# Performance work log

Measured on AMD Instinct MI355X. Metric: run time of the kernel, lower is better.

The kernel has to match this reference:

```python
import jax, jax.numpy as jnp
import numpy as np

N_NODES = 50000
N_EDGES = 800000


def _glorot(key, shape):
    fan_in, fan_out = shape
    lim = float(np.sqrt(6.0 / (fan_in + fan_out)))
    return jax.random.uniform(key, shape, jnp.float32, -lim, lim)


def setup_inputs() -> dict:
    key = jax.random.key(0)
    ks = jax.random.split(key, 8)
    x = jax.random.normal(ks[0], (N_NODES, 2), jnp.float32)
    edge_index = jax.random.randint(ks[1], (2, N_EDGES), 0, N_NODES, jnp.int64)
    edge_weight = jax.random.uniform(ks[2], (N_EDGES,), jnp.float32)
    return {
        "x": x,
        "edge_index": edge_index,
        "edge_weight": edge_weight,
        "W1": _glorot(ks[3], (2, 128)),
        "b1": jnp.zeros((128,), jnp.float32),
        "W2": _glorot(ks[4], (128, 64)),
        "b2": jnp.zeros((64,), jnp.float32),
        "W3": _glorot(ks[5], (64, 1)),
        "b3": jnp.zeros((1,), jnp.float32),
    }


def _gcn_conv(x, W, b, src, dst, ew, n_nodes):
    # PyG GCNConv with normalize=False: out[i] = sum_{e:(j->i)} ew[e] * (x_j @ W) + b
    h = x @ W                       # [N, F_out] tiny GEMM
    msg = h[src] * ew[:, None]      # [E, F_out] gather + scale
    out = jax.ops.segment_sum(msg, dst, num_segments=n_nodes)  # scatter-add
    return out + b


def reference(x, edge_index, edge_weight, W1, b1, W2, b2, W3, b3):
    src, dst = edge_index[0], edge_index[1]  # source_to_target flow: aggregate at dst
    n = x.shape[0]
    h1 = jax.nn.relu(_gcn_conv(x, W1, b1, src, dst, edge_weight, n))
    # dropout is a no-op in eval mode
    h2 = jax.nn.relu(_gcn_conv(h1, W2, b2, src, dst, edge_weight, n))
    h3 = _gcn_conv(h2, W3, b3, src, dst, edge_weight, n)  # [N, 1]
    return h3.squeeze(-1)  # [N]
```

## Files before the change

### kernel.cpp

```cpp
#include <hip/hip_runtime.h>
#include <hip/hip_fp16.h>

#define N_NODES 50000
#define N_EDGES 800000
#define BSHIFT 7
#define NBKT ((N_NODES + 127) >> BSHIFT)
#define CAP 3072
#define P1_EDGES 2048
#define P1_BLOCKS ((N_EDGES + P1_EDGES - 1) / P1_EDGES)
#define BIN_THREADS 512
#define SL_THREADS 512

__global__ void bin_edges(const int* __restrict__ src, const int* __restrict__ dst,
                          const float* __restrict__ ew, int* __restrict__ bcur,
                          unsigned* __restrict__ bpk, unsigned char* __restrict__ bdl) {
    __shared__ unsigned spk[P1_EDGES];
    __shared__ unsigned short sdst[P1_EDGES];
    __shared__ int cnt[NBKT];
    __shared__ int cbase[NBKT];
    int t = threadIdx.x;
    if (t < NBKT) cnt[t] = 0;
    __syncthreads();
    int e0 = blockIdx.x * P1_EDGES;
    for (int k = 0; k < P1_EDGES / BIN_THREADS; k++) {
        int i = k * BIN_THREADS + t;
        int e = e0 + i;
        if (e < N_EDGES) {
            int d = dst[e];
            unsigned hw = (unsigned)__half_as_ushort(__float2half(ew[e]));
            spk[i] = (unsigned)src[e] | (hw << 16);
            sdst[i] = (unsigned short)d;
            atomicAdd(&cnt[d >> BSHIFT], 1);
        }
    }
    __syncthreads();
    if (t < NBKT) {
        int v = cnt[t];
        int base = v ? atomicAdd(&bcur[t], v) : 0;
        cbase[t] = t * CAP + base;
        cnt[t] = 0;
    }
    __syncthreads();
    int nmax = N_EDGES - e0;
    if (nmax > P1_EDGES) nmax = P1_EDGES;
    for (int k = 0; k < P1_EDGES / BIN_THREADS; k++) {
        int i = k * BIN_THREADS + t;
        if (i < nmax) {
            int d = sdst[i];
            int b = d >> BSHIFT;
            int pos = cbase[b] + atomicAdd(&cnt[b], 1);
            bpk[pos] = spk[i];
            bdl[pos] = (unsigned char)(d & 127);
        }
    }
}

__device__ __forceinline__ float edge_w(unsigned p) {
    return __half2float(__ushort_as_half((unsigned short)(p >> 16)));
}

typedef _Float16 f16x8 __attribute__((ext_vector_type(8)));
typedef float f32x4 __attribute__((ext_vector_type(4)));

__global__ __launch_bounds__(SL_THREADS) void sort_l1(
    const int* __restrict__ bcur, const unsigned* __restrict__ bpk,
    const unsigned char* __restrict__ bdl, const float* __restrict__ x,
    const float* __restrict__ W1, const float* __restrict__ b1,
    const float* __restrict__ W2,
    unsigned* __restrict__ sorted, int2* __restrict__ rowspan,
    __half* __restrict__ t2) {
    __shared__ unsigned spk[CAP];
    __shared__ unsigned short sdl[CAP];
    __shared__ int nh[128], scn[128], lcur[128];
    __shared__ float nodeA[128], nodeB[128];
    __shared__ __align__(16) __half w2t[64][136];
    __shared__ __align__(16) float w1r0[128];
    __shared__ __align__(16) float w1r1[128];
    __shared__ __align__(16) float b1s[128];

    int b = blockIdx.x;
    int t = threadIdx.x;
    int base = b * CAP;
    int n = bcur[b];
    if (n > CAP) n = CAP;

    for (int idx = t; idx < 128 * 64; idx += SL_THREADS) {
        int k = idx >> 6, nn = idx & 63;
        w2t[nn][k] = __float2half(W2[idx]);
    }
    if (t < 128) {
        w1r0[t] = W1[t];
        w1r1[t] = W1[128 + t];
        b1s[t]  = b1[t];
        nh[t] = 0;
        lcur[t] = 0;
        nodeA[t] = 0.f;
        nodeB[t] = 0.f;
    }
    __syncthreads();

    for (int e = t; e < n; e += SL_THREADS) {
        spk[e] = bpk[base + e];
        unsigned short d = bdl[base + e];
        sdl[e] = d;
        atomicAdd(&nh[d], 1);
    }
    __syncthreads();

    int v = 0;
    if (t < 128) { v = nh[t]; scn[t] = v; }
    __syncthreads();
    for (int off = 1; off < 128; off <<= 1) {
        int u = (t < 128 && t >= off) ? scn[t - off] : 0;
        __syncthreads();
        if (t < 128) scn[t] += u;
        __syncthreads();
    }
    if (t < 128) {
        int ex = scn[t] - v;
        int node = (b << BSHIFT) + t;
        if (node < N_NODES) rowspan[node] = make_int2(base + ex, base + ex + v);
        nh[t] = ex;
    }
    __syncthreads();

    for (int e = t; e < n; e += SL_THREADS) {
        unsigned p = spk[e];
        int dlow = sdl[e];
        int pos = base + nh[dlow] + atomicAdd(&lcur[dlow], 1);
        sorted[pos] = p;
        float w = edge_w(p);
        float2 xv = ((const float2*)x)[p & 0xFFFF];
        atomicAdd(&nodeA[dlow], w * xv.x);
        atomicAdd(&nodeB[dlow], w * xv.y);
    }
    __syncthreads();

    int wave = t >> 6, lane = t & 63;
    int m0 = wave * 16;
    int fr = lane & 15;
    int kb = (lane >> 4) * 8;
    float a0 = nodeA[m0 + fr];
    float a1 = nodeB[m0 + fr];
    f32x4 acc0 = {0.f, 0.f, 0.f, 0.f};
    f32x4 acc1 = {0.f, 0.f, 0.f, 0.f};
    f32x4 acc2 = {0.f, 0.f, 0.f, 0.f};
    f32x4 acc3 = {0.f, 0.f, 0.f, 0.f};
#pragma unroll
    for (int k0 = 0; k0 < 128; k0 += 32) {
        f16x8 av;
#pragma unroll
        for (int j = 0; j < 8; j++) {
            int k = k0 + kb + j;
            float h = fmaxf(fmaf(a0, w1r0[k], fmaf(a1, w1r1[k], b1s[k])), 0.f);
            av[j] = (_Float16)h;
        }
        f16x8 bv0 = *(const f16x8*)&w2t[ 0 + fr][k0 + kb];
        f16x8 bv1 = *(const f16x8*)&w2t[16 + fr][k0 + kb];
        f16x8 bv2 = *(const f16x8*)&w2t[32 + fr][k0 + kb];
        f16x8 bv3 = *(const f16x8*)&w2t[48 + fr][k0 + kb];
        acc0 = __builtin_amdgcn_mfma_f32_16x16x32_f16(av, bv0, acc0, 0, 0, 0);
        acc1 = __builtin_amdgcn_mfma_f32_16x16x32_f16(av, bv1, acc1, 0, 0, 0);
        acc2 = __builtin_amdgcn_mfma_f32_16x16x32_f16(av, bv2, acc2, 0, 0, 0);
        acc3 = __builtin_amdgcn_mfma_f32_16x16x32_f16(av, bv3, acc3, 0, 0, 0);
    }
    int rowb = (b << BSHIFT) + m0 + (lane >> 4) * 4;
#pragma unroll
    for (int r = 0; r < 4; r++) {
        int node = rowb + r;
        if (node < N_NODES) {
            __half* o = t2 + node * 64 + fr;
            o[0]  = __float2half(acc0[r]);
            o[16] = __float2half(acc1[r]);
            o[32] = __float2half(acc2[r]);
            o[48] = __float2half(acc3[r]);
        }
    }
}

__global__ void gather2_dot3(const int2* __restrict__ rowspan, const unsigned* __restrict__ sorted,
                             const __half* __restrict__ t2, const float* __restrict__ b2,
                             const float* __restrict__ W3, float* __restrict__ t3) {
    int gtid = blockIdx.x * blockDim.x + threadIdx.x;
    int node = gtid >> 6;
    int lane = threadIdx.x & 63;
    if (node >= N_NODES) return;
    int eg  = lane >> 3;
    int fli = lane & 7;
    int2 sp = rowspan[node];
    float a0 = 0.f, a1 = 0.f, a2 = 0.f, a3 = 0.f, a4 = 0.f, a5 = 0.f, a6 = 0.f, a7 = 0.f;
    int e = sp.x + eg;
    for (; e + 8 < sp.y; e += 16) {
        unsigned p0 = sorted[e];
        unsigned p1 = sorted[e + 8];
        uint4 q0 = *(const uint4*)(t2 + (p0 & 0xFFFF) * 64 + fli * 8);
        uint4 q1 = *(const uint4*)(t2 + (p1 & 0xFFFF) * 64 + fli * 8);
        float w0 = edge_w(p0), w1 = edge_w(p1);
        float2 f;
        f = __half22float2(*(const __half2*)&q0.x); a0 = fmaf(w0, f.x, a0); a1 = fmaf(w0, f.y, a1);
        f = __half22float2(*(const __half2*)&q0.y); a2 = fmaf(w0, f.x, a2); a3 = fmaf(w0, f.y, a3);
        f = __half22float2(*(const __half2*)&q0.z); a4 = fmaf(w0, f.x, a4); a5 = fmaf(w0, f.y, a5);
        f = __half22float2(*(const __half2*)&q0.w); a6 = fmaf(w0, f.x, a6); a7 = fmaf(w0, f.y, a7);
        f = __half22float2(*(const __half2*)&q1.x); a0 = fmaf(w1, f.x, a0); a1 = fmaf(w1, f.y, a1);
        f = __half22float2(*(const __half2*)&q1.y); a2 = fmaf(w1, f.x, a2); a3 = fmaf(w1, f.y, a3);
        f = __half22float2(*(const __half2*)&q1.z); a4 = fmaf(w1, f.x, a4); a5 = fmaf(w1, f.y, a5);
        f = __half22float2(*(const __half2*)&q1.w); a6 = fmaf(w1, f.x, a6); a7 = fmaf(w1, f.y, a7);
    }
    if (e < sp.y) {
        unsigned p = sorted[e];
        uint4 q = *(const uint4*)(t2 + (p & 0xFFFF) * 64 + fli * 8);
        float w = edge_w(p);
        float2 f;
        f = __half22float2(*(const __half2*)&q.x); a0 = fmaf(w, f.x, a0); a1 = fmaf(w, f.y, a1);
        f = __half22float2(*(const __half2*)&q.y); a2 = fmaf(w, f.x, a2); a3 = fmaf(w, f.y, a3);
        f = __half22float2(*(const __half2*)&q.z); a4 = fmaf(w, f.x, a4); a5 = fmaf(w, f.y, a5);
        f = __half22float2(*(const __half2*)&q.w); a6 = fmaf(w, f.x, a6); a7 = fmaf(w, f.y, a7);
    }
#pragma unroll
    for (int off = 8; off < 64; off <<= 1) {
        a0 += __shfl_xor(a0, off); a1 += __shfl_xor(a1, off);
        a2 += __shfl_xor(a2, off); a3 += __shfl_xor(a3, off);
        a4 += __shfl_xor(a4, off); a5 += __shfl_xor(a5, off);
        a6 += __shfl_xor(a6, off); a7 += __shfl_xor(a7, off);
    }
    float4 bA = *(const float4*)(b2 + fli * 8);
    float4 bB = *(const float4*)(b2 + fli * 8 + 4);
    float4 wA = *(const float4*)(W3 + fli * 8);
    float4 wB = *(const float4*)(W3 + fli * 8 + 4);
    float h = fmaxf(a0 + bA.x, 0.f) * wA.x + fmaxf(a1 + bA.y, 0.f) * wA.y +
              fmaxf(a2 + bA.z, 0.f) * wA.z + fmaxf(a3 + bA.w, 0.f) * wA.w +
              fmaxf(a4 + bB.x, 0.f) * wB.x + fmaxf(a5 + bB.y, 0.f) * wB.y +
              fmaxf(a6 + bB.z, 0.f) * wB.z + fmaxf(a7 + bB.w, 0.f) * wB.w;
#pragma unroll
    for (int off = 1; off < 8; off <<= 1) h += __shfl_xor(h, off);
    if (lane == 0) t3[node] = h;
}

__global__ void gather3(const int2* __restrict__ rowspan, const unsigned* __restrict__ sorted,
                        const float* __restrict__ t3, const float* __restrict__ b3,
                        float* __restrict__ out) {
    int gtid = blockIdx.x * blockDim.x + threadIdx.x;
    int wid = gtid >> 6;
    int lane = threadIdx.x & 63;
    int sub = lane >> 4;
    int sl  = lane & 15;
    int node = wid * 4 + sub;
    if (node >= N_NODES) return;
    int2 sp = rowspan[node];
    float acc = 0.f;
    for (int e = sp.x + sl; e < sp.y; e += 16) {
        unsigned p = sorted[e];
        acc = fmaf(edge_w(p), t3[p & 0xFFFF], acc);
    }
#pragma unroll
    for (int off = 1; off < 16; off <<= 1) acc += __shfl_xor(acc, off);
    if (sl == 0) out[node] = acc + b3[0];
}

extern "C" void kernel_launch(void* const* d_in, const int* in_sizes, int n_in,
                              void* d_out, int out_size, void* d_ws, size_t ws_size,
                              hipStream_t stream) {
    const float* x  = (const float*)d_in[0];
    const int*   ei = (const int*)d_in[1];
    const float* ew = (const float*)d_in[2];
    const float* W1 = (const float*)d_in[3];
    const float* b1 = (const float*)d_in[4];
    const float* W2 = (const float*)d_in[5];
    const float* b2 = (const float*)d_in[6];
    const float* W3 = (const float*)d_in[7];
    const float* b3 = (const float*)d_in[8];
    float* out = (float*)d_out;

    const int* src = ei;
    const int* dst = ei + N_EDGES;

    char* p = (char*)d_ws;
    int*  bcur    = (int*)p;            p += NBKT * sizeof(int);
    p = (char*)(((uintptr_t)p + 15) & ~(uintptr_t)15);
    int2* rowspan = (int2*)p;           p += N_NODES * sizeof(int2);
    unsigned* bpk = (unsigned*)p;       p += (long)NBKT * CAP * sizeof(unsigned);
    unsigned char* bdl = (unsigned char*)p; p += (long)NBKT * CAP;
    p = (char*)(((uintptr_t)p + 15) & ~(uintptr_t)15);
    unsigned* sorted  = (unsigned*)p;   p += (long)NBKT * CAP * sizeof(unsigned);
    __half* t2    = (__half*)p;         p += 64L * N_NODES * sizeof(__half);
    float* t3     = (float*)p;          p += N_NODES * sizeof(float);

    hipMemsetAsync(bcur, 0, NBKT * sizeof(int), stream);

    bin_edges<<<P1_BLOCKS, BIN_THREADS, 0, stream>>>(src, dst, ew, bcur, bpk, bdl);

    sort_l1<<<NBKT, SL_THREADS, 0, stream>>>(bcur, bpk, bdl, x, W1, b1, W2, sorted, rowspan, t2);

    gather2_dot3<<<(N_NODES * 64 + 255) / 256, 256, 0, stream>>>(rowspan, sorted, t2, b2, W3, t3);

    gather3<<<((N_NODES + 3) / 4 * 64 + 255) / 256, 256, 0, stream>>>(rowspan, sorted, t3, b3, out);
}
```

Before: 146.8 us.

## Stage binned edges locally in shared memory for coalesced bucket writes

The bin_edges kernel now sorts each tile's edges by bucket in shared memory, using a prefix scan over bucket counts, before writing to global memory. Writes to each bucket become contiguous runs instead of scattered stores, and the separate packed-key and low-destination arrays are merged into one uint2 record. The cost is more shared memory and an extra scan and pass in binning, and each record grows from 5 to 8 bytes. The launch uses NBKT (391) blocks, which matches the previous P1_BLOCKS value.

```diff
diff --git a/kernel.cpp b/kernel.cpp
--- a/kernel.cpp
+++ b/kernel.cpp
@@ -4,67 +4,80 @@
 #define N_NODES 50000
 #define N_EDGES 800000
 #define BSHIFT 7
-#define NBKT ((N_NODES + 127) >> BSHIFT)
+#define NBKT 391
 #define CAP 3072
-#define P1_EDGES 2048
-#define P1_BLOCKS ((N_EDGES + P1_EDGES - 1) / P1_EDGES)
+#define TILE 2048
 #define BIN_THREADS 512
 #define SL_THREADS 512
 
-__global__ void bin_edges(const int* __restrict__ src, const int* __restrict__ dst,
-                          const float* __restrict__ ew, int* __restrict__ bcur,
-                          unsigned* __restrict__ bpk, unsigned char* __restrict__ bdl) {
-    __shared__ unsigned spk[P1_EDGES];
-    __shared__ unsigned short sdst[P1_EDGES];
-    __shared__ int cnt[NBKT];
-    __shared__ int cbase[NBKT];
-    int t = threadIdx.x;
-    if (t < NBKT) cnt[t] = 0;
-    __syncthreads();
-    int e0 = blockIdx.x * P1_EDGES;
-    for (int k = 0; k < P1_EDGES / BIN_THREADS; k++) {
-        int i = k * BIN_THREADS + t;
-        int e = e0 + i;
-        if (e < N_EDGES) {
-            int d = dst[e];
-            unsigned hw = (unsigned)__half_as_ushort(__float2half(ew[e]));
-            spk[i] = (unsigned)src[e] | (hw << 16);
-            sdst[i] = (unsigned short)d;
-            atomicAdd(&cnt[d >> BSHIFT], 1);
-        }
-    }
-    __syncthreads();
-    if (t < NBKT) {
-        int v = cnt[t];
-        int base = v ? atomicAdd(&bcur[t], v) : 0;
-        cbase[t] = t * CAP + base;
-        cnt[t] = 0;
-    }
-    __syncthreads();
-    int nmax = N_EDGES - e0;
-    if (nmax > P1_EDGES) nmax = P1_EDGES;
-    for (int k = 0; k < P1_EDGES / BIN_THREADS; k++) {
-        int i = k * BIN_THREADS + t;
-        if (i < nmax) {
-            int d = sdst[i];
-            int b = d >> BSHIFT;
-            int pos = cbase[b] + atomicAdd(&cnt[b], 1);
-            bpk[pos] = spk[i];
-            bdl[pos] = (unsigned char)(d & 127);
-        }
-    }
-}
+typedef _Float16 f16x8 __attribute__((ext_vector_type(8)));
+typedef float f32x4 __attribute__((ext_vector_type(4)));
 
 __device__ __forceinline__ float edge_w(unsigned p) {
     return __half2float(__ushort_as_half((unsigned short)(p >> 16)));
 }
 
-typedef _Float16 f16x8 __attribute__((ext_vector_type(8)));
-typedef float f32x4 __attribute__((ext_vector_type(4)));
+__global__ __launch_bounds__(BIN_THREADS) void bin_edges(
+    const int* __restrict__ src, const int* __restrict__ dstA,
+    const float* __restrict__ ew, int* __restrict__ bcur,
+    uint2* __restrict__ brec) {
+    __shared__ unsigned pk[TILE];
+    __shared__ unsigned short sdst[TILE];
+    __shared__ uint2 rec[TILE];
+    __shared__ int cnt[NBKT];
+    __shared__ int lofs[NBKT];
+    __shared__ int cbase[NBKT];
+    __shared__ int scn[BIN_THREADS];
+
+    int t = threadIdx.x;
+    int e0 = blockIdx.x * TILE;
+    int nmax = N_EDGES - e0;
+    if (nmax > TILE) nmax = TILE;
+    if (nmax < 0) nmax = 0;
+    if (t < NBKT) cnt[t] = 0;
+    __syncthreads();
+    for (int i = t; i < nmax; i += BIN_THREADS) {
+        int e = e0 + i;
+        int d = dstA[e];
+        unsigned hw = (unsigned)__half_as_ushort(__float2half(ew[e]));
+        pk[i] = (unsigned)src[e] | (hw << 16);
+        sdst[i] = (unsigned short)d;
+        atomicAdd(&cnt[d >> BSHIFT], 1);
+    }
+    __syncthreads();
+    int v = (t < NBKT) ? cnt[t] : 0;
+    scn[t] = v;
+    __syncthreads();
+    for (int off = 1; off < BIN_THREADS; off <<= 1) {
+        int u = (t >= off) ? scn[t - off] : 0;
+        __syncthreads();
+        scn[t] += u;
+        __syncthreads();
+    }
+    if (t < NBKT) {
+        lofs[t] = scn[t] - v;
+        cbase[t] = t * CAP + (v ? atomicAdd(&bcur[t], v) : 0);
+        cnt[t] = 0;
+    }
+    __syncthreads();
+    for (int i = t; i < nmax; i += BIN_THREADS) {
+        int d = sdst[i];
+        int bk = d >> BSHIFT;
+        int pos = lofs[bk] + atomicAdd(&cnt[bk], 1);
+        rec[pos] = make_uint2(pk[i], (unsigned)d);
+    }
+    __syncthreads();
+    for (int i = t; i < nmax; i += BIN_THREADS) {
+        uint2 r = rec[i];
+        int bk = (int)(r.y >> BSHIFT);
+        int g = cbase[bk] + (i - lofs[bk]);
+        brec[g] = r;
+    }
+}
 
 __global__ __launch_bounds__(SL_THREADS) void sort_l1(
-    const int* __restrict__ bcur, const unsigned* __restrict__ bpk,
-    const unsigned char* __restrict__ bdl, const float* __restrict__ x,
+    const int* __restrict__ bcur, const uint2* __restrict__ brec,
+    const float* __restrict__ x,
     const float* __restrict__ W1, const float* __restrict__ b1,
     const float* __restrict__ W2,
     unsigned* __restrict__ sorted, int2* __restrict__ rowspan,
@@ -100,15 +113,16 @@
     __syncthreads();
 
     for (int e = t; e < n; e += SL_THREADS) {
-        spk[e] = bpk[base + e];
-        unsigned short d = bdl[base + e];
-        sdl[e] = d;
+        uint2 r = brec[base + e];
+        spk[e] = r.x;
+        int d = (int)(r.y & 127u);
+        sdl[e] = (unsigned short)d;
         atomicAdd(&nh[d], 1);
     }
     __syncthreads();
 
-    int v = 0;
-    if (t < 128) { v = nh[t]; scn[t] = v; }
+    int vv = 0;
+    if (t < 128) { vv = nh[t]; scn[t] = vv; }
     __syncthreads();
     for (int off = 1; off < 128; off <<= 1) {
         int u = (t < 128 && t >= off) ? scn[t - off] : 0;
@@ -117,9 +131,9 @@
         __syncthreads();
     }
     if (t < 128) {
-        int ex = scn[t] - v;
+        int ex = scn[t] - vv;
         int node = (b << BSHIFT) + t;
-        if (node < N_NODES) rowspan[node] = make_int2(base + ex, base + ex + v);
+        if (node < N_NODES) rowspan[node] = make_int2(base + ex, base + ex + vv);
         nh[t] = ex;
     }
     __syncthreads();
@@ -278,18 +292,16 @@
     int*  bcur    = (int*)p;            p += NBKT * sizeof(int);
     p = (char*)(((uintptr_t)p + 15) & ~(uintptr_t)15);
     int2* rowspan = (int2*)p;           p += N_NODES * sizeof(int2);
-    unsigned* bpk = (unsigned*)p;       p += (long)NBKT * CAP * sizeof(unsigned);
-    unsigned char* bdl = (unsigned char*)p; p += (long)NBKT * CAP;
-    p = (char*)(((uintptr_t)p + 15) & ~(uintptr_t)15);
-    unsigned* sorted  = (unsigned*)p;   p += (long)NBKT * CAP * sizeof(unsigned);
+    uint2* brec   = (uint2*)p;          p += (long)NBKT * CAP * sizeof(uint2);
+    unsigned* sorted = (unsigned*)p;    p += (long)NBKT * CAP * sizeof(unsigned);
     __half* t2    = (__half*)p;         p += 64L * N_NODES * sizeof(__half);
     float* t3     = (float*)p;          p += N_NODES * sizeof(float);
 
     hipMemsetAsync(bcur, 0, NBKT * sizeof(int), stream);
 
-    bin_edges<<<P1_BLOCKS, BIN_THREADS, 0, stream>>>(src, dst, ew, bcur, bpk, bdl);
-
-    sort_l1<<<NBKT, SL_THREADS, 0, stream>>>(bcur, bpk, bdl, x, W1, b1, W2, sorted, rowspan, t2);
+    bin_edges<<<NBKT, BIN_THREADS, 0, stream>>>(src, dst, ew, bcur, brec);
+
+    sort_l1<<<NBKT, SL_THREADS, 0, stream>>>(bcur, brec, x, W1, b1, W2, sorted, rowspan, t2);
 
     gather2_dot3<<<(N_NODES * 64 + 255) / 256, 256, 0, stream>>>(rowspan, sorted, t2, b2, W3, t3);
 
```

Result: faster. 141.9 us (-3.3%).
